# Kernel tuning notes

Measured on AMD Instinct MI355X. Metric: run time of the kernel, lower is better.

The kernel has to match this reference:

```python
import jax, jax.numpy as jnp
import numpy as np

INPUT_DIM = 1024
HIDDEN_DIM = 2048
NUM_BLOCKS = 8
BLOCK_SIZE = HIDDEN_DIM // NUM_BLOCKS
BATCH = 2048


def setup_inputs() -> dict:
    key = jax.random.key(0)
    ks = jax.random.split(key, 6)
    # PyTorch GRUCell init: uniform(-1/sqrt(hidden_size), 1/sqrt(hidden_size))
    bound = 1.0 / np.sqrt(BLOCK_SIZE)
    u = lambda k, shape: jax.random.uniform(k, shape, jnp.float32, -bound, bound)
    return {
        "input": jax.random.normal(ks[0], (BATCH, INPUT_DIM), jnp.float32),
        "hidden": jax.random.normal(ks[1], (BATCH, HIDDEN_DIM), jnp.float32),
        # stacked per-block GRUCell params (block-diagonal structure)
        "W_ih": u(ks[2], (NUM_BLOCKS, 3 * BLOCK_SIZE, INPUT_DIM)),
        "W_hh": u(ks[3], (NUM_BLOCKS, 3 * BLOCK_SIZE, BLOCK_SIZE)),
        "b_ih": u(ks[4], (NUM_BLOCKS, 3 * BLOCK_SIZE)),
        "b_hh": u(ks[5], (NUM_BLOCKS, 3 * BLOCK_SIZE)),
    }


def reference(input, hidden, W_ih, W_hh, b_ih, b_hh):
    B = input.shape[0]
    nb, g3, bs = W_hh.shape  # [num_blocks, 3*block_size, block_size]
    hb = hidden.reshape(B, nb, bs)                      # [B, nb, bs]
    # input-to-gate and hidden-to-gate projections, batched over blocks
    gi = jnp.einsum("bi,ngi->bng", input, W_ih) + b_ih  # [B, nb, 3*bs]
    gh = jnp.einsum("bns,ngs->bng", hb, W_hh) + b_hh    # [B, nb, 3*bs]
    i_r, i_z, i_n = jnp.split(gi, 3, axis=-1)
    h_r, h_z, h_n = jnp.split(gh, 3, axis=-1)
    r = jax.nn.sigmoid(i_r + h_r)
    z = jax.nn.sigmoid(i_z + h_z)
    n = jnp.tanh(i_n + r * h_n)
    new_h = (1.0 - z) * n + z * hb                      # [B, nb, bs]
    return new_h.reshape(B, nb * bs)
```

## Files before the change

### kernel.cpp

```cpp
#include <hip/hip_runtime.h>
#include <hip/hip_bf16.h>
#include <type_traits>

typedef __attribute__((ext_vector_type(4))) float f32x4;
typedef __attribute__((ext_vector_type(8))) short bf16x8;

template <int V> using ic = std::integral_constant<int, V>;

static constexpr int B_   = 2048;
static constexpr int IN_  = 1024;
static constexpr int HID_ = 2048;
static constexpr int NB_  = 8;
static constexpr int BS_  = 256;
static constexpr int G3_  = 768;

__device__ __forceinline__ unsigned cvtpk(float lo, float hi) {
  unsigned r;
  asm("v_cvt_pk_bf16_f32 %0, %1, %2" : "=v"(r) : "v"(lo), "v"(hi));
  return r;
}

__global__ __launch_bounds__(256, 2) void gru_mfma(
    const float* __restrict__ xf,
    const float* __restrict__ hf,
    const float* __restrict__ Wih,
    const float* __restrict__ Whh,
    const float* __restrict__ b_ih,
    const float* __restrict__ b_hh,
    float* __restrict__ out)
{
  __shared__ __align__(16) char lds[2][20480];

  const int t    = threadIdx.x;
  const int lane = t & 63;
  const int wid  = t >> 6;
  const int wm   = wid >> 1;
  const int wn   = wid & 1;

  const int bid = blockIdx.x;
  const int swz = (bid & 7) * 64 + (bid >> 3);
  const int mrow0 = (swz & 15) * 128;
  const int ct    = swz >> 4;
  const int n     = ct >> 2;
  const int s0    = (ct & 3) * 64;

  int arow[2], acolE[2];
#pragma unroll
  for (int p = 0; p < 2; ++p) {
    int op = p * 4096 + t * 16;
    int ol = op ^ (((op >> 6) & 3) << 4);
    arow[p]  = ol >> 6;
    acolE[p] = (ol & 63) >> 1;
  }
  int wgrow[3], wcolE[3];
#pragma unroll
  for (int q = 0; q < 3; ++q) {
    int op = q * 4096 + t * 16;
    int ol = op ^ (((op >> 6) & 3) << 4);
    int wr = ol >> 6;
    wgrow[q]  = n * G3_ + (wr >> 6) * BS_ + s0 + (wr & 63);
    wcolE[q]  = (ol & 63) >> 1;
  }

  f32x4 acc[4][4][2] = {};
  float4 sa[2][2];
  float4 sw[3][2];

  auto issue = [&](int tt) {
#pragma unroll
    for (int p = 0; p < 2; ++p) {
      const float* src = (tt < 32)
        ? xf + (size_t)(mrow0 + arow[p]) * IN_  + tt * 32 + acolE[p]
        : hf + (size_t)(mrow0 + arow[p]) * HID_ + n * BS_ + (tt - 32) * 32 + acolE[p];
      sa[p][0] = *reinterpret_cast<const float4*>(src);
      sa[p][1] = *reinterpret_cast<const float4*>(src + 4);
    }
#pragma unroll
    for (int q = 0; q < 3; ++q) {
      const float* src = (tt < 32)
        ? Wih + (size_t)wgrow[q] * IN_ + tt * 32 + wcolE[q]
        : Whh + (size_t)wgrow[q] * BS_ + (tt - 32) * 32 + wcolE[q];
      sw[q][0] = *reinterpret_cast<const float4*>(src);
      sw[q][1] = *reinterpret_cast<const float4*>(src + 4);
    }
  };
  auto pack8 = [&](const float4& a, const float4& b) {
    union { unsigned u[4]; bf16x8 v; } r;
    r.u[0] = cvtpk(a.x, a.y); r.u[1] = cvtpk(a.z, a.w);
    r.u[2] = cvtpk(b.x, b.y); r.u[3] = cvtpk(b.z, b.w);
    return r.v;
  };
  auto writeAll = [&](int buf) {
    char* base = (char*)lds[buf];
#pragma unroll
    for (int p = 0; p < 2; ++p)
      *reinterpret_cast<bf16x8*>(base + p * 4096 + t * 16) = pack8(sa[p][0], sa[p][1]);
#pragma unroll
    for (int q = 0; q < 3; ++q)
      *reinterpret_cast<bf16x8*>(base + 8192 + q * 4096 + t * 16) = pack8(sw[q][0], sw[q][1]);
  };

  auto compute = [&](int buf, auto ph1c) {
    constexpr bool PH1 = decltype(ph1c)::value;
    const char* base = (const char*)lds[buf];
    bf16x8 af[4];
#pragma unroll
    for (int mi = 0; mi < 4; ++mi) {
      int ar  = wm * 64 + mi * 16 + (lane & 15);
      int off = (ar * 64 + ((lane >> 4) * 16)) ^ ((ar & 3) << 4);
      af[mi] = *reinterpret_cast<const bf16x8*>(base + off);
    }
    __builtin_amdgcn_s_setprio(1);
#pragma unroll
    for (int g = 0; g < 3; ++g) {
      bf16x8 wf[2];
#pragma unroll
      for (int ni = 0; ni < 2; ++ni) {
        int wr  = g * 64 + wn * 32 + ni * 16 + (lane & 15);
        int off = (wr * 64 + ((lane >> 4) * 16)) ^ ((wr & 3) << 4);
        wf[ni] = *reinterpret_cast<const bf16x8*>(base + 8192 + off);
      }
      constexpr int set2 = PH1 ? 2 : 3;
      const int set = (g < 2) ? g : set2;
#pragma unroll
      for (int mi = 0; mi < 4; ++mi)
#pragma unroll
        for (int ni = 0; ni < 2; ++ni)
          acc[set][mi][ni] = __builtin_amdgcn_mfma_f32_16x16x32_bf16(
              af[mi], wf[ni], acc[set][mi][ni], 0, 0, 0);
    }
    __builtin_amdgcn_s_setprio(0);
  };

  issue(0);
  writeAll(0);
  __syncthreads();

#pragma unroll
  for (int tt = 0; tt < 40; ++tt) {
    const int cur = tt & 1;

    if (tt < 39) issue(tt + 1);
    __builtin_amdgcn_sched_barrier(0);
    if (tt < 32) compute(cur, std::true_type{});
    else         compute(cur, std::false_type{});
    __builtin_amdgcn_sched_barrier(0);
    if (tt < 39) writeAll(cur ^ 1);
    __syncthreads();
  }

#pragma unroll
  for (int ni = 0; ni < 2; ++ni) {
    int scol = s0 + wn * 32 + ni * 16 + (lane & 15);
    float br_i = b_ih[n * G3_ + 0 * BS_ + scol];
    float bz_i = b_ih[n * G3_ + 1 * BS_ + scol];
    float bn_i = b_ih[n * G3_ + 2 * BS_ + scol];
    float br_h = b_hh[n * G3_ + 0 * BS_ + scol];
    float bz_h = b_hh[n * G3_ + 1 * BS_ + scol];
    float bn_h = b_hh[n * G3_ + 2 * BS_ + scol];
    int gcol = n * BS_ + scol;
#pragma unroll
    for (int mi = 0; mi < 4; ++mi) {
#pragma unroll
      for (int i = 0; i < 4; ++i) {
        int row = mrow0 + wm * 64 + mi * 16 + (lane >> 4) * 4 + i;
        float hprev = hf[(size_t)row * HID_ + gcol];
        float rr = acc[0][mi][ni][i] + br_i + br_h;
        float zz = acc[1][mi][ni][i] + bz_i + bz_h;
        float r  = 1.f / (1.f + __expf(-rr));
        float z  = 1.f / (1.f + __expf(-zz));
        float ng = tanhf(acc[2][mi][ni][i] + bn_i + r * (acc[3][mi][ni][i] + bn_h));
        out[(size_t)row * HID_ + gcol] = (1.f - z) * ng + z * hprev;
      }
    }
  }
}

extern "C" void kernel_launch(void* const* d_in, const int* in_sizes, int n_in,
                              void* d_out, int out_size, void* d_ws, size_t ws_size,
                              hipStream_t stream) {
  const float* x   = (const float*)d_in[0];
  const float* h   = (const float*)d_in[1];
  const float* Wih = (const float*)d_in[2];
  const float* Whh = (const float*)d_in[3];
  const float* bih = (const float*)d_in[4];
  const float* bhh = (const float*)d_in[5];
  float* out = (float*)d_out;
  (void)d_ws; (void)ws_size;

  gru_mfma<<<512, 256, 0, stream>>>(x, h, Wih, Whh, bih, bhh, out);
}
```

Before: 52.57 us.

## Use two-level XOR LDS swizzle and LDS-staged vectorized epilogue stores

Changes the LDS swizzle to XOR in bits from the next row group as well, aiming to reduce bank conflicts on the MFMA fragment reads. The epilogue now stages the z and n gate values in LDS per wave and then reads hidden and writes output as float4 rows instead of scattered scalar accesses, so global memory traffic is better coalesced. The cost is extra LDS traffic and waitcnt barriers in the epilogue. The per-wave staging relies on wave-local ordering and reuses the pipeline buffers after the final sync.

```diff
diff --git a/kernel.cpp b/kernel.cpp
--- a/kernel.cpp
+++ b/kernel.cpp
@@ -4,8 +4,6 @@
 
 typedef __attribute__((ext_vector_type(4))) float f32x4;
 typedef __attribute__((ext_vector_type(8))) short bf16x8;
-
-template <int V> using ic = std::integral_constant<int, V>;
 
 static constexpr int B_   = 2048;
 static constexpr int IN_  = 1024;
@@ -48,7 +46,8 @@
 #pragma unroll
   for (int p = 0; p < 2; ++p) {
     int op = p * 4096 + t * 16;
-    int ol = op ^ (((op >> 6) & 3) << 4);
+    int sx = ((op >> 6) & 3) ^ ((op >> 8) & 3);
+    int ol = op ^ (sx << 4);
     arow[p]  = ol >> 6;
     acolE[p] = (ol & 63) >> 1;
   }
@@ -56,7 +55,8 @@
 #pragma unroll
   for (int q = 0; q < 3; ++q) {
     int op = q * 4096 + t * 16;
-    int ol = op ^ (((op >> 6) & 3) << 4);
+    int sx = ((op >> 6) & 3) ^ ((op >> 8) & 3);
+    int ol = op ^ (sx << 4);
     int wr = ol >> 6;
     wgrow[q]  = n * G3_ + (wr >> 6) * BS_ + s0 + (wr & 63);
     wcolE[q]  = (ol & 63) >> 1;
@@ -106,8 +106,9 @@
     bf16x8 af[4];
 #pragma unroll
     for (int mi = 0; mi < 4; ++mi) {
-      int ar  = wm * 64 + mi * 16 + (lane & 15);
-      int off = (ar * 64 + ((lane >> 4) * 16)) ^ ((ar & 3) << 4);
+      int ar = wm * 64 + mi * 16 + (lane & 15);
+      int sg = (ar & 3) ^ ((ar >> 2) & 3);
+      int off = ar * 64 + ((((lane >> 4)) ^ sg) << 4);
       af[mi] = *reinterpret_cast<const bf16x8*>(base + off);
     }
     __builtin_amdgcn_s_setprio(1);
@@ -116,8 +117,9 @@
       bf16x8 wf[2];
 #pragma unroll
       for (int ni = 0; ni < 2; ++ni) {
-        int wr  = g * 64 + wn * 32 + ni * 16 + (lane & 15);
-        int off = (wr * 64 + ((lane >> 4) * 16)) ^ ((wr & 3) << 4);
+        int wr = g * 64 + wn * 32 + ni * 16 + (lane & 15);
+        int sg = (wr & 3) ^ ((wr >> 2) & 3);
+        int off = wr * 64 + ((((lane >> 4)) ^ sg) << 4);
         wf[ni] = *reinterpret_cast<const bf16x8*>(base + 8192 + off);
       }
       constexpr int set2 = PH1 ? 2 : 3;
@@ -149,29 +151,57 @@
     __syncthreads();
   }
 
-#pragma unroll
-  for (int ni = 0; ni < 2; ++ni) {
-    int scol = s0 + wn * 32 + ni * 16 + (lane & 15);
-    float br_i = b_ih[n * G3_ + 0 * BS_ + scol];
-    float bz_i = b_ih[n * G3_ + 1 * BS_ + scol];
-    float bn_i = b_ih[n * G3_ + 2 * BS_ + scol];
-    float br_h = b_hh[n * G3_ + 0 * BS_ + scol];
-    float bz_h = b_hh[n * G3_ + 1 * BS_ + scol];
-    float bn_h = b_hh[n * G3_ + 2 * BS_ + scol];
-    int gcol = n * BS_ + scol;
-#pragma unroll
-    for (int mi = 0; mi < 4; ++mi) {
-#pragma unroll
-      for (int i = 0; i < 4; ++i) {
-        int row = mrow0 + wm * 64 + mi * 16 + (lane >> 4) * 4 + i;
-        float hprev = hf[(size_t)row * HID_ + gcol];
-        float rr = acc[0][mi][ni][i] + br_i + br_h;
-        float zz = acc[1][mi][ni][i] + bz_i + bz_h;
-        float r  = 1.f / (1.f + __expf(-rr));
-        float z  = 1.f / (1.f + __expf(-zz));
-        float ng = tanhf(acc[2][mi][ni][i] + bn_i + r * (acc[3][mi][ni][i] + bn_h));
-        out[(size_t)row * HID_ + gcol] = (1.f - z) * ng + z * hprev;
+  float* ew = (float*)lds + wid * 2304;
+  const int gc0 = n * BS_ + s0 + wn * 32;
+
+#pragma unroll
+  for (int half = 0; half < 2; ++half) {
+#pragma unroll
+    for (int ml = 0; ml < 2; ++ml) {
+      const int mi = half * 2 + ml;
+#pragma unroll
+      for (int ni = 0; ni < 2; ++ni) {
+        int scol = s0 + wn * 32 + ni * 16 + (lane & 15);
+        float br_i = b_ih[n * G3_ + 0 * BS_ + scol];
+        float bz_i = b_ih[n * G3_ + 1 * BS_ + scol];
+        float bn_i = b_ih[n * G3_ + 2 * BS_ + scol];
+        float br_h = b_hh[n * G3_ + 0 * BS_ + scol];
+        float bz_h = b_hh[n * G3_ + 1 * BS_ + scol];
+        float bn_h = b_hh[n * G3_ + 2 * BS_ + scol];
+#pragma unroll
+        for (int i = 0; i < 4; ++i) {
+          float rr = acc[0][mi][ni][i] + br_i + br_h;
+          float zz = acc[1][mi][ni][i] + bz_i + bz_h;
+          float r  = 1.f / (1.f + __expf(-rr));
+          float z  = 1.f / (1.f + __expf(-zz));
+          float ng = tanhf(acc[2][mi][ni][i] + bn_i + r * (acc[3][mi][ni][i] + bn_h));
+          int lrow = ml * 16 + (lane >> 4) * 4 + i;
+          int lcol = ni * 16 + (lane & 15);
+          ew[lrow * 72 + lcol]      = z;
+          ew[lrow * 72 + 36 + lcol] = ng;
+        }
       }
+    }
+    asm volatile("s_waitcnt lgkmcnt(0)");
+    __builtin_amdgcn_sched_barrier(0);
+#pragma unroll
+    for (int p = 0; p < 4; ++p) {
+      int lrow = p * 8 + (lane >> 3);
+      int grow = mrow0 + wm * 64 + half * 32 + lrow;
+      int cc   = (lane & 7) * 4;
+      float4 z4  = *reinterpret_cast<const float4*>(ew + lrow * 72 + cc);
+      float4 ng4 = *reinterpret_cast<const float4*>(ew + lrow * 72 + 36 + cc);
+      float4 h4  = *reinterpret_cast<const float4*>(hf + (size_t)grow * HID_ + gc0 + cc);
+      float4 o4;
+      o4.x = (1.f - z4.x) * ng4.x + z4.x * h4.x;
+      o4.y = (1.f - z4.y) * ng4.y + z4.y * h4.y;
+      o4.z = (1.f - z4.z) * ng4.z + z4.z * h4.z;
+      o4.w = (1.f - z4.w) * ng4.w + z4.w * h4.w;
+      *reinterpret_cast<float4*>(out + (size_t)grow * HID_ + gc0 + cc) = o4;
+    }
+    if (half == 0) {
+      asm volatile("s_waitcnt lgkmcnt(0)");
+      __builtin_amdgcn_sched_barrier(0);
     }
   }
 }
```

Result: no change. 52.83 us (+0.5%).
